# Kernel tuning notes

Measured on AMD Instinct MI355X. Metric: run time of the kernel, lower is better.

## Reference

```python
import jax, jax.numpy as jnp
import numpy as np

EPS = 1e-5
N_HEADS = 16
TOP_K = 2


def _ln(x, g, b):
    m = x.mean(-1, keepdims=True)
    v = ((x - m) ** 2).mean(-1, keepdims=True)
    return (x - m) / jnp.sqrt(v + EPS) * g + b


def _block_fwd(x, ln1_g, ln1_b, ln2_g, ln2_b, Wq, bq, Wk, bk, Wv, bv, Wo, bo,
               Wr, br, e_w1, e_b1, e_w2, e_b2):
    B, S, D = x.shape
    H = N_HEADS
    hd = D // H
    # --- LN + causal MHA + residual (dropout is identity at eval) ---
    h = _ln(x, ln1_g, ln1_b)
    q = (h @ Wq + bq).reshape(B, S, H, hd).transpose(0, 2, 1, 3)  # [B,H,S,hd]
    k = (h @ Wk + bk).reshape(B, S, H, hd).transpose(0, 2, 1, 3)
    v = (h @ Wv + bv).reshape(B, S, H, hd).transpose(0, 2, 1, 3)
    scores = jnp.einsum('bhqd,bhkd->bhqk', q, k) / (hd ** 0.5)
    causal = jnp.tril(jnp.ones((S, S), dtype=bool))
    scores = jnp.where(causal, scores, -jnp.inf)
    attn = jax.nn.softmax(scores, axis=-1)
    o = jnp.einsum('bhqk,bhkd->bhqd', attn, v).transpose(0, 2, 1, 3).reshape(B, S, D)
    a = (o @ Wo + bo) + x
    # --- LN + dense-computed SparseMoE + residual ---
    h2 = _ln(a, ln2_g, ln2_b)
    logits = h2 @ Wr + br                         # [B,S,E]
    topv = jax.lax.top_k(logits, TOP_K)[0]        # [B,S,K]
    kmask = logits >= topv[..., -1:]
    w = jax.nn.softmax(jnp.where(kmask, logits, -jnp.inf), axis=-1)  # [B,S,E]
    # dense per-expert FFN, exactly as the torch module computes it
    mid = jax.nn.gelu(jnp.einsum('bsd,edf->bsef', h2, e_w1) + e_b1,
                      approximate=False)          # [B,S,E,4D]
    eo = jnp.einsum('bsef,efd->bsed', mid, e_w2) + e_b2  # [B,S,E,D]
    moe = jnp.einsum('bse,bsed->bsd', w, eo)
    return moe + a


def setup_inputs() -> dict:
    key = jax.random.key(0)
    B, S, D, E = 1, 2048, 1024, 8
    F = 4 * D
    ks = jax.random.split(key, 8)

    def n(k, shape):
        return jax.random.normal(k, shape, jnp.float32) * 0.02

    return dict(
        x=jax.random.normal(ks[0], (B, S, D), jnp.float32),
        ln1_g=jnp.ones((D,), jnp.float32), ln1_b=jnp.zeros((D,), jnp.float32),
        ln2_g=jnp.ones((D,), jnp.float32), ln2_b=jnp.zeros((D,), jnp.float32),
        Wq=n(ks[1], (D, D)), bq=jnp.zeros((D,), jnp.float32),
        Wk=n(ks[2], (D, D)), bk=jnp.zeros((D,), jnp.float32),
        Wv=n(ks[3], (D, D)), bv=jnp.zeros((D,), jnp.float32),
        Wo=n(ks[4], (D, D)), bo=jnp.zeros((D,), jnp.float32),
        Wr=n(ks[5], (D, E)), br=jnp.zeros((E,), jnp.float32),
        e_w1=n(ks[6], (E, D, F)), e_b1=jnp.zeros((E, F), jnp.float32),
        e_w2=n(ks[7], (E, F, D)), e_b2=jnp.zeros((E, D), jnp.float32),
    )


def reference(x, ln1_g, ln1_b, ln2_g, ln2_b, Wq, bq, Wk, bk, Wv, bv, Wo, bo,
              Wr, br, e_w1, e_b1, e_w2, e_b2):
    return _block_fwd(x, ln1_g, ln1_b, ln2_g, ln2_b, Wq, bq, Wk, bk, Wv, bv,
                      Wo, bo, Wr, br, e_w1, e_b1, e_w2, e_b2)
```

## Files before the change

kernel.cpp:

```cpp
#include <hip/hip_runtime.h>
#include <hip/hip_bf16.h>
#include <math.h>

#define S 2048
#define Dm 1024
#define Ee 8
#define Ff 4096

typedef __attribute__((ext_vector_type(8))) short bf16x8;
typedef __attribute__((ext_vector_type(4))) float f32x4;

__device__ __forceinline__ unsigned short f2bf(float f) {
    union { float f; unsigned int u; } c; c.f = f;
    unsigned int r = (c.u + 0x7fffu + ((c.u >> 16) & 1u)) >> 16;
    return (unsigned short)r;
}

__device__ __forceinline__ void gload16(const void* g, void* l) {
    __builtin_amdgcn_global_load_lds(
        (const __attribute__((address_space(1))) void*)g,
        (__attribute__((address_space(3))) void*)l, 16, 0, 0);
}

__device__ __forceinline__ float gelu_f(float x) {
    float ax = fabsf(x) * 0.70710678118654752f;
    float t = 1.0f / (1.0f + 0.3275911f * ax);
    float p = t * (0.254829592f + t * (-0.284496736f + t * (1.421413741f +
              t * (-1.453152027f + t * 1.061405429f))));
    float er = 1.0f - p * __expf(-ax * ax);
    er = (x < 0.0f) ? -er : er;
    return 0.5f * x * (1.0f + er);
}

__global__ __launch_bounds__(256) void ln_kernel(const float* __restrict__ x,
                                                 const float* __restrict__ g,
                                                 const float* __restrict__ b,
                                                 unsigned short* __restrict__ obf) {
    int row = blockIdx.x;
    int tid = threadIdx.x;
    float4 v = ((const float4*)(x + (size_t)row * Dm))[tid];
    float s  = v.x + v.y + v.z + v.w;
    float sq = v.x*v.x + v.y*v.y + v.z*v.z + v.w*v.w;
    #pragma unroll
    for (int off = 1; off < 64; off <<= 1) {
        s  += __shfl_xor(s, off);
        sq += __shfl_xor(sq, off);
    }
    __shared__ float ps[4], pq[4];
    int wave = tid >> 6;
    if ((tid & 63) == 0) { ps[wave] = s; pq[wave] = sq; }
    __syncthreads();
    s  = ps[0] + ps[1] + ps[2] + ps[3];
    sq = pq[0] + pq[1] + pq[2] + pq[3];
    float mean = s * (1.0f / Dm);
    float var  = sq * (1.0f / Dm) - mean * mean;
    float rstd = rsqrtf(var + 1e-5f);
    float4 gv = ((const float4*)g)[tid];
    float4 bv = ((const float4*)b)[tid];
    float4 o;
    o.x = (v.x - mean) * rstd * gv.x + bv.x;
    o.y = (v.y - mean) * rstd * gv.y + bv.y;
    o.z = (v.z - mean) * rstd * gv.z + bv.z;
    o.w = (v.w - mean) * rstd * gv.w + bv.w;
    unsigned short t4[4] = { f2bf(o.x), f2bf(o.y), f2bf(o.z), f2bf(o.w) };
    *(uint2*)(obf + (size_t)row * Dm + tid * 4) = *(uint2*)t4;
}

__global__ __launch_bounds__(256) void ln2_fused(const float* __restrict__ x,
                                                 const float* __restrict__ p0,
                                                 const float* __restrict__ p1,
                                                 const float* __restrict__ bo,
                                                 const float* __restrict__ g,
                                                 const float* __restrict__ b,
                                                 const float* __restrict__ Wr,
                                                 const float* __restrict__ br,
                                                 float* __restrict__ aout,
                                                 unsigned short* __restrict__ h2b,
                                                 float* __restrict__ w_rt) {
    int row = blockIdx.x;
    int tid = threadIdx.x;
    size_t base = (size_t)row * Dm;
    float4 xv = ((const float4*)(x + base))[tid];
    float4 a0 = ((const float4*)(p0 + base))[tid];
    float4 a1 = ((const float4*)(p1 + base))[tid];
    float4 bv0 = ((const float4*)bo)[tid];
    float4 a;
    a.x = xv.x + a0.x + a1.x + bv0.x;
    a.y = xv.y + a0.y + a1.y + bv0.y;
    a.z = xv.z + a0.z + a1.z + bv0.z;
    a.w = xv.w + a0.w + a1.w + bv0.w;
    ((float4*)(aout + base))[tid] = a;
    float s  = a.x + a.y + a.z + a.w;
    float sq = a.x*a.x + a.y*a.y + a.z*a.z + a.w*a.w;
    #pragma unroll
    for (int off = 1; off < 64; off <<= 1) {
        s  += __shfl_xor(s, off);
        sq += __shfl_xor(sq, off);
    }
    __shared__ float ps[4], pq[4];
    int wave = tid >> 6;
    if ((tid & 63) == 0) { ps[wave] = s; pq[wave] = sq; }
    __syncthreads();
    s  = ps[0] + ps[1] + ps[2] + ps[3];
    sq = pq[0] + pq[1] + pq[2] + pq[3];
    float mean = s * (1.0f / Dm);
    float var  = sq * (1.0f / Dm) - mean * mean;
    float rstd = rsqrtf(var + 1e-5f);
    float4 gv = ((const float4*)g)[tid];
    float4 bbv = ((const float4*)b)[tid];
    float4 o;
    o.x = (a.x - mean) * rstd * gv.x + bbv.x;
    o.y = (a.y - mean) * rstd * gv.y + bbv.y;
    o.z = (a.z - mean) * rstd * gv.z + bbv.z;
    o.w = (a.w - mean) * rstd * gv.w + bbv.w;
    unsigned short t4[4] = { f2bf(o.x), f2bf(o.y), f2bf(o.z), f2bf(o.w) };
    *(uint2*)(h2b + base + tid * 4) = *(uint2*)t4;

    float lg[8];
    #pragma unroll
    for (int e = 0; e < 8; e++) lg[e] = 0.0f;
    float oc[4] = { o.x, o.y, o.z, o.w };
    #pragma unroll
    for (int c = 0; c < 4; c++) {
        const float4* wr4 = (const float4*)(Wr + (size_t)(tid * 4 + c) * Ee);
        float4 wa = wr4[0], wb = wr4[1];
        lg[0] += oc[c]*wa.x; lg[1] += oc[c]*wa.y; lg[2] += oc[c]*wa.z; lg[3] += oc[c]*wa.w;
        lg[4] += oc[c]*wb.x; lg[5] += oc[c]*wb.y; lg[6] += oc[c]*wb.z; lg[7] += oc[c]*wb.w;
    }
    #pragma unroll
    for (int e = 0; e < 8; e++)
        #pragma unroll
        for (int off = 1; off < 64; off <<= 1) lg[e] += __shfl_xor(lg[e], off);
    __shared__ float wlg[4][8];
    if ((tid & 63) == 0) {
        #pragma unroll
        for (int e = 0; e < 8; e++) wlg[wave][e] = lg[e];
    }
    __syncthreads();
    if (tid == 0) {
        float l8[8];
        #pragma unroll
        for (int e = 0; e < 8; e++) l8[e] = wlg[0][e] + wlg[1][e] + wlg[2][e] + wlg[3][e] + br[e];
        float v1 = -INFINITY, v2 = -INFINITY;
        for (int e = 0; e < 8; e++) {
            float xv2 = l8[e];
            if (xv2 > v1) { v2 = v1; v1 = xv2; }
            else if (xv2 > v2) v2 = xv2;
        }
        float wv[8]; float denom = 0.0f;
        for (int e = 0; e < 8; e++) {
            if (l8[e] >= v2) { wv[e] = __expf(l8[e] - v1); denom += wv[e]; }
            else wv[e] = 0.0f;
        }
        float inv = 1.0f / denom;
        for (int e = 0; e < 8; e++) w_rt[row * Ee + e] = wv[e] * inv;
    }
}

__global__ __launch_bounds__(256) void tconv(const float* __restrict__ src,
                                             unsigned short* __restrict__ dst,
                                             int Kk, int Nn) {
    src += (size_t)blockIdx.z * Kk * Nn;
    dst += (size_t)blockIdx.z * Kk * Nn;
    int n0 = blockIdx.x * 64, k0 = blockIdx.y * 64;
    int tid = threadIdx.x;
    __shared__ float t[64][65];
    #pragma unroll
    for (int p = 0; p < 4; p++) {
        int kr = p * 16 + (tid >> 4);
        int nc = (tid & 15) * 4;
        float4 v = *(const float4*)(src + (size_t)(k0 + kr) * Nn + n0 + nc);
        t[kr][nc] = v.x; t[kr][nc+1] = v.y; t[kr][nc+2] = v.z; t[kr][nc+3] = v.w;
    }
    __syncthreads();
    int nr = tid >> 2;
    int kc = (tid & 3) * 16;
    unsigned short o[16];
    #pragma unroll
    for (int j = 0; j < 16; j++) o[j] = f2bf(t[kc + j][nr]);
    *(bf16x8*)(dst + (size_t)(n0 + nr) * Kk + k0 + kc)     = *(bf16x8*)&o[0];
    *(bf16x8*)(dst + (size_t)(n0 + nr) * Kk + k0 + kc + 8) = *(bf16x8*)&o[8];
}

template<int MODE>
__global__ __launch_bounds__(256, 2) void gemm_db(const unsigned short* __restrict__ A,
                                                  const unsigned short* __restrict__ Wt,
                                                  const float* __restrict__ bias0,
                                                  const float* __restrict__ bias1,
                                                  const float* __restrict__ bias2,
                                                  void* __restrict__ Cout,
                                                  int M, int N, int K) {
    const int tid = threadIdx.x;
    const int lane = tid & 63;
    const int w = tid >> 6;
    const int lr = lane >> 4, lc = lane & 15;
    const int wr = w >> 1, wc = w & 1;

    int kc = (MODE == 1) ? blockIdx.z : 0;
    const int m0 = blockIdx.y * 128;
    const int n0 = blockIdx.x * 128;
    const int KL   = (MODE == 1) ? 512 : K;
    const int Koff = kc * KL;

    __shared__ __align__(16) unsigned short As[2][128 * 64];
    __shared__ __align__(16) unsigned short Bs[2][128 * 64];

    const int srow = lane >> 3;
    const int csw  = ((lane & 7) ^ srow) * 8;
    const unsigned short* asrc[4];
    const unsigned short* bsrc[4];
    #pragma unroll
    for (int i = 0; i < 4; i++) {
        int rl = w * 32 + i * 8 + srow;
        asrc[i] = A  + (size_t)(m0 + rl) * K + Koff + csw;
        bsrc[i] = Wt + (size_t)(n0 + rl) * K + Koff + csw;
    }

    f32x4 acc[4][4];
    #pragma unroll
    for (int a = 0; a < 4; a++)
        #pragma unroll
        for (int bb = 0; bb < 4; bb++) acc[a][bb] = (f32x4)0.0f;

    auto STAGE = [&](int buf, int kblk) {
        const size_t koff = (size_t)kblk * 64;
        #pragma unroll
        for (int i = 0; i < 4; i++) {
            gload16(asrc[i] + koff, &As[buf][(w * 32 + i * 8) * 64]);
            gload16(bsrc[i] + koff, &Bs[buf][(w * 32 + i * 8) * 64]);
        }
    };

    const int nt = KL / 64;
    STAGE(0, 0);
    for (int t = 0; t < nt; ++t) {
        const int cur = t & 1;
        if (t + 1 < nt) {
            STAGE(cur ^ 1, t + 1);
            asm volatile("s_waitcnt vmcnt(8)" ::: "memory");
        } else {
            asm volatile("s_waitcnt vmcnt(0)" ::: "memory");
        }
        __builtin_amdgcn_s_barrier();
        #pragma unroll
        for (int ks = 0; ks < 2; ks++) {
            const int ck = ((ks * 4 + lr) ^ (lc & 7)) * 8;
            bf16x8 af[4], bfv[4];
            #pragma unroll
            for (int fm = 0; fm < 4; fm++)
                af[fm] = *(const bf16x8*)&As[cur][(wr * 64 + fm * 16 + lc) * 64 + ck];
            #pragma unroll
            for (int fn = 0; fn < 4; fn++)
                bfv[fn] = *(const bf16x8*)&Bs[cur][(wc * 64 + fn * 16 + lc) * 64 + ck];
            #pragma unroll
            for (int fm = 0; fm < 4; fm++)
                #pragma unroll
                for (int fn = 0; fn < 4; fn++)
                    acc[fm][fn] = __builtin_amdgcn_mfma_f32_16x16x32_bf16(af[fm], bfv[fn], acc[fm][fn], 0, 0, 0);
        }
        asm volatile("" ::: "memory");
        __builtin_amdgcn_s_barrier();
    }

    #pragma unroll
    for (int fm = 0; fm < 4; fm++) {
        #pragma unroll
        for (int r = 0; r < 4; r++) {
            int m = m0 + wr * 64 + fm * 16 + lr * 4 + r;
            #pragma unroll
            for (int fn = 0; fn < 4; fn++) {
                int ncol = n0 + wc * 64 + fn * 16 + lc;
                float val = acc[fm][fn][r];
                if constexpr (MODE == 0) {
                    const float* bb = (ncol < 1024) ? bias0 : (ncol < 2048 ? bias1 : bias2);
                    val += bb[ncol & 1023];
                    ((unsigned short*)Cout)[(size_t)m * N + ncol] = f2bf(val);
                } else {
                    ((float*)Cout)[(size_t)kc * M * N + (size_t)m * N + ncol] = val;
                }
            }
        }
    }
}

template<int MODE>
__global__ __launch_bounds__(256, 4) void gemm_moe(const unsigned short* __restrict__ A,
                                                   const unsigned short* __restrict__ Wt,
                                                   const float* __restrict__ bias,
                                                   void* __restrict__ Cout,
                                                   const int* __restrict__ rows,
                                                   const int* __restrict__ counts,
                                                   const int* __restrict__ offs,
                                                   int N, int K) {
    const int tid = threadIdx.x;
    const int lane = tid & 63;
    const int w = tid >> 6;
    const int lr = lane >> 4, lc = lane & 15;
    const int wr = w >> 1, wc = w & 1;

    int e, kc;
    if constexpr (MODE == 2) { e = blockIdx.z; kc = 0; }
    else { e = blockIdx.z >> 2; kc = blockIdx.z & 3; }
    const int Mcnt = counts[e];
    const int m0 = blockIdx.y * 128;
    if (m0 >= Mcnt) return;
    const int n0 = blockIdx.x * 128;
    const int KL = (MODE == 3) ? (K >> 2) : K;
    const int Koff = kc * KL;
    const unsigned short* Wz = Wt + (size_t)e * N * K;
    const float* biasz = bias + (size_t)e * N;
    const int zoff = offs[e];

    __shared__ __align__(16) unsigned short As[128 * 64];
    __shared__ __align__(16) unsigned short Bs[128 * 64];

    const int srow = lane >> 3;
    const int csw  = ((lane & 7) ^ srow) * 8;
    const unsigned short* asrc[4];
    const unsigned short* bsrc[4];
    #pragma unroll
    for (int i = 0; i < 4; i++) {
        int rl = w * 32 + i * 8 + srow;
        int ma = m0 + rl;
        int srcRow;
        if constexpr (MODE == 2) srcRow = rows[e * S + (ma < Mcnt ? ma : Mcnt - 1)];
        else                     srcRow = zoff + (ma < Mcnt ? ma : Mcnt - 1);
        asrc[i] = A  + (size_t)srcRow * K + Koff + csw;
        bsrc[i] = Wz + (size_t)(n0 + rl) * K + Koff + csw;
    }

    f32x4 acc[4][4];
    #pragma unroll
    for (int a = 0; a < 4; a++)
        #pragma unroll
        for (int bb = 0; bb < 4; bb++) acc[a][bb] = (f32x4)0.0f;

    for (int k0 = 0; k0 < KL; k0 += 64) {
        #pragma unroll
        for (int i = 0; i < 4; i++) {
            gload16(asrc[i] + k0, &As[(w * 32 + i * 8) * 64]);
            gload16(bsrc[i] + k0, &Bs[(w * 32 + i * 8) * 64]);
        }
        __syncthreads();
        #pragma unroll
        for (int ks = 0; ks < 2; ks++) {
            const int ck = ((ks * 4 + lr) ^ (lc & 7)) * 8;
            bf16x8 af[4], bfv[4];
            #pragma unroll
            for (int fm = 0; fm < 4; fm++)
                af[fm] = *(const bf16x8*)&As[(wr * 64 + fm * 16 + lc) * 64 + ck];
            #pragma unroll
            for (int fn = 0; fn < 4; fn++)
                bfv[fn] = *(const bf16x8*)&Bs[(wc * 64 + fn * 16 + lc) * 64 + ck];
            #pragma unroll
            for (int fm = 0; fm < 4; fm++)
                #pragma unroll
                for (int fn = 0; fn < 4; fn++)
                    acc[fm][fn] = __builtin_amdgcn_mfma_f32_16x16x32_bf16(af[fm], bfv[fn], acc[fm][fn], 0, 0, 0);
        }
        __syncthreads();
    }

    #pragma unroll
    for (int fm = 0; fm < 4; fm++) {
        #pragma unroll
        for (int r = 0; r < 4; r++) {
            int m = m0 + wr * 64 + fm * 16 + lr * 4 + r;
            if (m >= Mcnt) continue;
            #pragma unroll
            for (int fn = 0; fn < 4; fn++) {
                int ncol = n0 + wc * 64 + fn * 16 + lc;
                float val = acc[fm][fn][r];
                if constexpr (MODE == 2) {
                    val += biasz[ncol];
                    ((unsigned short*)Cout)[(size_t)(zoff + m) * N + ncol] = f2bf(gelu_f(val));
                } else {
                    if (kc == 0) val += biasz[ncol];
                    ((float*)Cout)[(size_t)kc * 4096 * N + (size_t)(zoff + m) * N + ncol] = val;
                }
            }
        }
    }
}

__global__ __launch_bounds__(256) void attn_mfma(const unsigned short* __restrict__ qkv,
                                                 unsigned short* __restrict__ ob) {
    int qt = (int)gridDim.x - 1 - (int)blockIdx.x;
    int h  = blockIdx.y;
    int tid = threadIdx.x;
    int lane = tid & 63, w = tid >> 6;
    int lr = lane >> 4, lc = lane & 15;

    __shared__ __align__(16) unsigned short Kl[2][64 * 64];
    __shared__ __align__(16) unsigned short Vt[2][64 * 64];
    __shared__ __align__(16) unsigned short Pl[4][16 * 64];

    bf16x8 qf[2];
    int qg_base = qt * 64 + w * 16;
    {
        int qrow = qg_base + lc;
        #pragma unroll
        for (int ks = 0; ks < 2; ks++)
            qf[ks] = *(const bf16x8*)(qkv + (size_t)qrow * 3072 + h * 64 + ks * 32 + lr * 8);
    }

    const int srow = lane >> 3;
    const int scw  = ((lane & 7) ^ srow) * 8;
    const unsigned short* ksrc[2];
    #pragma unroll
    for (int i = 0; i < 2; i++)
        ksrc[i] = qkv + (size_t)(w * 16 + i * 8 + srow) * 3072 + h * 64 + 1024 + scw;
    int vrow[2], vcg[2];
    const unsigned short* vsrc[2];
    #pragma unroll
    for (int i = 0; i < 2; i++) {
        int u = tid + i * 256;
        vrow[i] = u >> 3; vcg[i] = (u & 7) * 8;
        vsrc[i] = qkv + (size_t)vrow[i] * 3072 + h * 64 + 2048 + vcg[i];
    }

    f32x4 oacc[4];
    #pragma unroll
    for (int fd = 0; fd < 4; fd++) oacc[fd] = (f32x4)0.0f;
    float mrun[4], lrun[4];
    #pragma unroll
    for (int r = 0; r < 4; r++) { mrun[r] = -INFINITY; lrun[r] = 0.0f; }

    bf16x8 vreg[2];
    vreg[0] = *(const bf16x8*)(vsrc[0]);
    vreg[1] = *(const bf16x8*)(vsrc[1]);
    gload16(ksrc[0], &Kl[0][(w * 16 + 0) * 64]);
    gload16(ksrc[1], &Kl[0][(w * 16 + 8) * 64]);
    #pragma unroll
    for (int i = 0; i < 2; i++)
        #pragma unroll
        for (int j = 0; j < 8; j++) {
            int d = vcg[i] + j;
            int ch = ((vrow[i] >> 3) ^ (d & 7) ^ (d >> 3)) & 7;
            Vt[0][d * 64 + ch * 8 + (vrow[i] & 7)] = (unsigned short)vreg[i][j];
        }
    __syncthreads();

    for (int kt = 0; kt <= qt; kt++) {
        const int cur = kt & 1;
        if (kt < qt) {
            size_t off = (size_t)(kt + 1) * 64 * 3072;
            vreg[0] = *(const bf16x8*)(vsrc[0] + off);
            vreg[1] = *(const bf16x8*)(vsrc[1] + off);
            gload16(ksrc[0] + off, &Kl[cur ^ 1][(w * 16 + 0) * 64]);
            gload16(ksrc[1] + off, &Kl[cur ^ 1][(w * 16 + 8) * 64]);
        }

        f32x4 sc[4];
        #pragma unroll
        for (int fn = 0; fn < 4; fn++) sc[fn] = (f32x4)0.0f;
        #pragma unroll
        for (int fn = 0; fn < 4; fn++)
            #pragma unroll
            for (int ks = 0; ks < 2; ks++) {
                bf16x8 kf = *(const bf16x8*)&Kl[cur][(fn * 16 + lc) * 64 + ((ks * 4 + lr) ^ (lc & 7)) * 8];
                sc[fn] = __builtin_amdgcn_mfma_f32_16x16x32_bf16(qf[ks], kf, sc[fn], 0, 0, 0);
            }

        float st[4][4];
        float mloc[4];
        #pragma unroll
        for (int r = 0; r < 4; r++) mloc[r] = -INFINITY;
        #pragma unroll
        for (int fn = 0; fn < 4; fn++)
            #pragma unroll
            for (int r = 0; r < 4; r++) {
                float sv = sc[fn][r] * 0.125f;
                if (kt == qt) {
                    int kvg = kt * 64 + fn * 16 + lc;
                    int qg  = qg_base + lr * 4 + r;
                    if (kvg > qg) sv = -INFINITY;
                }
                st[fn][r] = sv;
                mloc[r] = fmaxf(mloc[r], sv);
            }
        #pragma unroll
        for (int r = 0; r < 4; r++) {
            mloc[r] = fmaxf(mloc[r], __shfl_xor(mloc[r], 1));
            mloc[r] = fmaxf(mloc[r], __shfl_xor(mloc[r], 2));
            mloc[r] = fmaxf(mloc[r], __shfl_xor(mloc[r], 4));
            mloc[r] = fmaxf(mloc[r], __shfl_xor(mloc[r], 8));
        }
        float fsc[4], lpart[4];
        #pragma unroll
        for (int r = 0; r < 4; r++) {
            float mnew = fmaxf(mrun[r], mloc[r]);
            fsc[r] = __expf(mrun[r] - mnew);
            mrun[r] = mnew;
            lpart[r] = 0.0f;
        }
        float pv[4][4];
        #pragma unroll
        for (int fn = 0; fn < 4; fn++)
            #pragma unroll
            for (int r = 0; r < 4; r++) {
                pv[fn][r] = __expf(st[fn][r] - mrun[r]);
                lpart[r] += pv[fn][r];
            }
        #pragma unroll
        for (int r = 0; r < 4; r++) {
            lpart[r] += __shfl_xor(lpart[r], 1);
            lpart[r] += __shfl_xor(lpart[r], 2);
            lpart[r] += __shfl_xor(lpart[r], 4);
            lpart[r] += __shfl_xor(lpart[r], 8);
            lrun[r] = lrun[r] * fsc[r] + lpart[r];
        }
        #pragma unroll
        for (int fn = 0; fn < 4; fn++)
            #pragma unroll
            for (int r = 0; r < 4; r++) {
                int q = lr * 4 + r;
                int kvc = fn * 16 + lc;
                int ch = ((kvc >> 3) ^ (q & 7) ^ (q >> 3)) & 7;
                Pl[w][q * 64 + ch * 8 + (kvc & 7)] = f2bf(pv[fn][r]);
            }
        #pragma unroll
        for (int fd = 0; fd < 4; fd++)
            #pragma unroll
            for (int r = 0; r < 4; r++) oacc[fd][r] *= fsc[r];

        if (kt < qt) {
            #pragma unroll
            for (int i = 0; i < 2; i++)
                #pragma unroll
                for (int j = 0; j < 8; j++) {
                    int d = vcg[i] + j;
                    int ch = ((vrow[i] >> 3) ^ (d & 7) ^ (d >> 3)) & 7;
                    Vt[cur ^ 1][d * 64 + ch * 8 + (vrow[i] & 7)] = (unsigned short)vreg[i][j];
                }
        }

        __syncthreads();

        #pragma unroll
        for (int ks = 0; ks < 2; ks++) {
            int chp = ((ks * 4 + lr) ^ (lc & 7) ^ (lc >> 3)) & 7;
            bf16x8 pa = *(const bf16x8*)&Pl[w][lc * 64 + chp * 8];
            #pragma unroll
            for (int fd = 0; fd < 4; fd++) {
                int d = fd * 16 + lc;
                int chv = ((ks * 4 + lr) ^ (d & 7) ^ (d >> 3)) & 7;
                bf16x8 vb = *(const bf16x8*)&Vt[cur][d * 64 + chv * 8];
                oacc[fd] = __builtin_amdgcn_mfma_f32_16x16x32_bf16(pa, vb, oacc[fd], 0, 0, 0);
            }
        }
        __syncthreads();
    }
    #pragma unroll
    for (int fd = 0; fd < 4; fd++)
        #pragma unroll
        for (int r = 0; r < 4; r++) {
            float val = oacc[fd][r] / lrun[r];
            ob[(size_t)(qg_base + lr * 4 + r) * 1024 + h * 64 + fd * 16 + lc] = f2bf(val);
        }
}

__global__ __launch_bounds__(256) void listbuild_kernel(const float* __restrict__ w_rt,
                                                        int* __restrict__ rows,
                                                        int* __restrict__ counts,
                                                        int* __restrict__ offs,
                                                        int* __restrict__ tok2slot,
                                                        float* __restrict__ tokw) {
    int tid = threadIdx.x;
    __shared__ int sc[256];
    __shared__ int runoff_s;
    int ncnt[8];
    #pragma unroll
    for (int j = 0; j < 8; j++) ncnt[j] = 0;
    if (tid == 0) runoff_s = 0;
    __syncthreads();
    for (int e = 0; e < Ee; e++) {
        int t0 = tid * 8;
        int sel = 0, flags = 0;
        #pragma unroll
        for (int j = 0; j < 8; j++)
            if (w_rt[(size_t)(t0 + j) * Ee + e] > 0.0f) { flags |= 1 << j; sel++; }
        sc[tid] = sel;
        __syncthreads();
        for (int off = 1; off < 256; off <<= 1) {
            int add = (tid >= off) ? sc[tid - off] : 0;
            __syncthreads();
            sc[tid] += add;
            __syncthreads();
        }
        int base = runoff_s;
        int pos = sc[tid] - sel;
        #pragma unroll
        for (int j = 0; j < 8; j++) {
            if (flags & (1 << j)) {
                rows[e * S + pos] = t0 + j;
                int c = ncnt[j];
                if (c < 2) {
                    tok2slot[(t0 + j) * 2 + c] = base + pos;
                    tokw[(t0 + j) * 2 + c] = w_rt[(size_t)(t0 + j) * Ee + e];
                    ncnt[j] = c + 1;
                }
                pos++;
            }
        }
        __syncthreads();
        if (tid == 0) {
            offs[e] = base;
            counts[e] = sc[255];
            runoff_s = base + sc[255];
        }
        __syncthreads();
    }
}

__global__ __launch_bounds__(256) void combine_kernel(float* __restrict__ out,
                                                      const float* __restrict__ eo,
                                                      const int* __restrict__ tok2slot,
                                                      const float* __restrict__ tokw) {
    int t = blockIdx.x, d = threadIdx.x;
    int s0 = tok2slot[t * 2], s1 = tok2slot[t * 2 + 1];
    float w0 = tokw[t * 2], w1 = tokw[t * 2 + 1];
    float4 o = ((const float4*)(out + (size_t)t * Dm))[d];
    float ax = 0, ay = 0, az = 0, aw = 0, bx = 0, by = 0, bz = 0, bw = 0;
    #pragma unroll
    for (int p = 0; p < 4; p++) {
        const float* ep = eo + (size_t)p * 4096 * Dm;
        float4 a = ((const float4*)(ep + (size_t)s0 * Dm))[d];
        float4 b = ((const float4*)(ep + (size_t)s1 * Dm))[d];
        ax += a.x; ay += a.y; az += a.z; aw += a.w;
        bx += b.x; by += b.y; bz += b.z; bw += b.w;
    }
    o.x += w0 * ax + w1 * bx;
    o.y += w0 * ay + w1 * by;
    o.z += w0 * az + w1 * bz;
    o.w += w0 * aw + w1 * bw;
    ((float4*)(out + (size_t)t * Dm))[d] = o;
}

extern "C" void kernel_launch(void* const* d_in, const int* in_sizes, int n_in,
                              void* d_out, int out_size, void* d_ws, size_t ws_size,
                              hipStream_t stream) {
    const float* x    = (const float*)d_in[0];
    const float* ln1g = (const float*)d_in[1];
    const float* ln1b = (const float*)d_in[2];
    const float* ln2g = (const float*)d_in[3];
    const float* ln2b = (const float*)d_in[4];
    const float* Wq   = (const float*)d_in[5];
    const float* bq   = (const float*)d_in[6];
    const float* Wk   = (const float*)d_in[7];
    const float* bk   = (const float*)d_in[8];
    const float* Wv   = (const float*)d_in[9];
    const float* bv   = (const float*)d_in[10];
    const float* Wo   = (const float*)d_in[11];
    const float* bo   = (const float*)d_in[12];
    const float* Wr   = (const float*)d_in[13];
    const float* br   = (const float*)d_in[14];
    const float* ew1  = (const float*)d_in[15];
    const float* eb1  = (const float*)d_in[16];
    const float* ew2  = (const float*)d_in[17];
    const float* eb2  = (const float*)d_in[18];
    float* out = (float*)d_out;

    char* wsb = (char*)d_ws;
    const size_t MB = 1 << 20;
    unsigned short* ew1T = (unsigned short*)(wsb);
    float*          eo   = (float*)         (wsb);
    unsigned short* ew2T = (unsigned short*)(wsb + 64*MB);
    unsigned short* mid  = (unsigned short*)(wsb + 128*MB);
    unsigned short* qkvT = (unsigned short*)(wsb + 160*MB);
    unsigned short* WoT  = (unsigned short*)(wsb + 166*MB);
    unsigned short* h_bf = (unsigned short*)(wsb + 168*MB);
    unsigned short* qkv  = (unsigned short*)(wsb + 172*MB);
    float*          p01  = (float*)         (wsb + 168*MB);
    unsigned short* ob   = (unsigned short*)(wsb + 184*MB);
    unsigned short* h2b  = (unsigned short*)(wsb + 196*MB);
    float*          w_rt = (float*)         (wsb + 200*MB);
    int*            rows = (int*)           (wsb + 200*MB + 65536);
    int*            counts   = rows + Ee * S;
    int*            offs     = counts + Ee;
    int*            tok2slot = offs + Ee;
    float*          tokw     = (float*)(tok2slot + 2 * S);

    tconv<<<dim3(16, 16, 1), 256, 0, stream>>>(Wq, qkvT,               Dm, Dm);
    tconv<<<dim3(16, 16, 1), 256, 0, stream>>>(Wk, qkvT + 1024*1024,   Dm, Dm);
    tconv<<<dim3(16, 16, 1), 256, 0, stream>>>(Wv, qkvT + 2*1024*1024, Dm, Dm);
    tconv<<<dim3(16, 16, 1), 256, 0, stream>>>(Wo, WoT,                Dm, Dm);
    tconv<<<dim3(64, 16, 8), 256, 0, stream>>>(ew1, ew1T, Dm, Ff);
    tconv<<<dim3(16, 64, 8), 256, 0, stream>>>(ew2, ew2T, Ff, Dm);

    ln_kernel<<<S, 256, 0, stream>>>(x, ln1g, ln1b, h_bf);

    gemm_db<0><<<dim3(24, 16), 256, 0, stream>>>(h_bf, qkvT, bq, bk, bv,
        qkv, S, 3072, Dm);

    attn_mfma<<<dim3(32, 16), 256, 0, stream>>>(qkv, ob);

    gemm_db<1><<<dim3(8, 16, 2), 256, 0, stream>>>(ob, WoT, nullptr, nullptr, nullptr,
        p01, S, Dm, Dm);

    ln2_fused<<<S, 256, 0, stream>>>(x, p01, p01 + (size_t)S * Dm, bo, ln2g, ln2b,
                                     Wr, br, out, h2b, w_rt);
    listbuild_kernel<<<1, 256, 0, stream>>>(w_rt, rows, counts, offs, tok2slot, tokw);

    gemm_moe<2><<<dim3(32, 16, 8), 256, 0, stream>>>(h2b, ew1T, eb1,
        mid, rows, counts, offs, Ff, Dm);

    gemm_moe<3><<<dim3(8, 16, 32), 256, 0, stream>>>(mid, ew2T, eb2,
        eo, rows, counts, offs, Dm, Ff);

    combine_kernel<<<S, 256, 0, stream>>>(out, eo, tok2slot, tokw);
}
```

Before: 395.3 us.

## Store MoE split-K partials as bf16, remap MoE blocks by XCD, rebalance attention grid

The second expert GEMM now writes its four split-K partial outputs as bf16 instead of fp32, and the combine kernel reads and widens them. This halves the traffic for that intermediate buffer but rounds each partial to bf16 before summation. The expert GEMM blocks are remapped so consecutive block ids stay on the same XCD, which aims to improve L2 reuse. The attention grid is flattened and interleaves descending and ascending query tiles across head halves to balance causal work. It also raises wave priority around the MFMA sections and drops one barrier that sat before the PV product.

```diff
diff --git a/kernel.cpp b/kernel.cpp
--- a/kernel.cpp
+++ b/kernel.cpp
@@ -14,6 +14,10 @@
     union { float f; unsigned int u; } c; c.f = f;
     unsigned int r = (c.u + 0x7fffu + ((c.u >> 16) & 1u)) >> 16;
     return (unsigned short)r;
+}
+
+__device__ __forceinline__ float bf2f(unsigned short u) {
+    union { float f; unsigned int i; } c; c.i = ((unsigned int)u) << 16; return c.f;
 }
 
 __device__ __forceinline__ void gload16(const void* g, void* l) {
@@ -298,13 +302,25 @@
     const int lr = lane >> 4, lc = lane & 15;
     const int wr = w >> 1, wc = w & 1;
 
+    const int nx = gridDim.x, ny = gridDim.y;
+    const int nwg = nx * ny * gridDim.z;
+    int b = (int)blockIdx.x + nx * ((int)blockIdx.y + ny * (int)blockIdx.z);
+    {
+        int q = nwg >> 3, r = nwg & 7;
+        int xcd = b & 7, idx = b >> 3;
+        b = ((xcd < r) ? xcd * (q + 1) : r * (q + 1) + (xcd - r) * q) + idx;
+    }
+    const int by = b % ny;
+    const int bx = (b / ny) % nx;
+    const int bz = b / (ny * nx);
+
     int e, kc;
-    if constexpr (MODE == 2) { e = blockIdx.z; kc = 0; }
-    else { e = blockIdx.z >> 2; kc = blockIdx.z & 3; }
+    if constexpr (MODE == 2) { e = bz; kc = 0; }
+    else { e = bz >> 2; kc = bz & 3; }
     const int Mcnt = counts[e];
-    const int m0 = blockIdx.y * 128;
+    const int m0 = by * 128;
     if (m0 >= Mcnt) return;
-    const int n0 = blockIdx.x * 128;
+    const int n0 = bx * 128;
     const int KL = (MODE == 3) ? (K >> 2) : K;
     const int Koff = kc * KL;
     const unsigned short* Wz = Wt + (size_t)e * N * K;
@@ -376,7 +392,7 @@
                     ((unsigned short*)Cout)[(size_t)(zoff + m) * N + ncol] = f2bf(gelu_f(val));
                 } else {
                     if (kc == 0) val += biasz[ncol];
-                    ((float*)Cout)[(size_t)kc * 4096 * N + (size_t)(zoff + m) * N + ncol] = val;
+                    ((unsigned short*)Cout)[(size_t)kc * 4096 * N + (size_t)(zoff + m) * N + ncol] = f2bf(val);
                 }
             }
         }
@@ -385,8 +401,10 @@
 
 __global__ __launch_bounds__(256) void attn_mfma(const unsigned short* __restrict__ qkv,
                                                  unsigned short* __restrict__ ob) {
-    int qt = (int)gridDim.x - 1 - (int)blockIdx.x;
-    int h  = blockIdx.y;
+    int bid = blockIdx.x;
+    int qt, h;
+    if (bid < 256) { qt = 31 - (bid & 31); h = bid >> 5; }
+    else           { qt = bid & 31;        h = 8 + ((bid - 256) >> 5); }
     int tid = threadIdx.x;
     int lane = tid & 63, w = tid >> 6;
     int lr = lane >> 4, lc = lane & 15;
@@ -454,6 +472,7 @@
         f32x4 sc[4];
         #pragma unroll
         for (int fn = 0; fn < 4; fn++) sc[fn] = (f32x4)0.0f;
+        __builtin_amdgcn_s_setprio(1);
         #pragma unroll
         for (int fn = 0; fn < 4; fn++)
             #pragma unroll
@@ -461,6 +480,7 @@
                 bf16x8 kf = *(const bf16x8*)&Kl[cur][(fn * 16 + lc) * 64 + ((ks * 4 + lr) ^ (lc & 7)) * 8];
                 sc[fn] = __builtin_amdgcn_mfma_f32_16x16x32_bf16(qf[ks], kf, sc[fn], 0, 0, 0);
             }
+        __builtin_amdgcn_s_setprio(0);
 
         float st[4][4];
         float mloc[4];
@@ -535,8 +555,7 @@
                 }
         }
 
-        __syncthreads();
-
+        __builtin_amdgcn_s_setprio(1);
         #pragma unroll
         for (int ks = 0; ks < 2; ks++) {
             int chp = ((ks * 4 + lr) ^ (lc & 7) ^ (lc >> 3)) & 7;
@@ -549,6 +568,7 @@
                 oacc[fd] = __builtin_amdgcn_mfma_f32_16x16x32_bf16(pa, vb, oacc[fd], 0, 0, 0);
             }
         }
+        __builtin_amdgcn_s_setprio(0);
         __syncthreads();
     }
     #pragma unroll
@@ -614,26 +634,28 @@
 }
 
 __global__ __launch_bounds__(256) void combine_kernel(float* __restrict__ out,
-                                                      const float* __restrict__ eo,
+                                                      const unsigned short* __restrict__ eo,
                                                       const int* __restrict__ tok2slot,
                                                       const float* __restrict__ tokw) {
     int t = blockIdx.x, d = threadIdx.x;
     int s0 = tok2slot[t * 2], s1 = tok2slot[t * 2 + 1];
     float w0 = tokw[t * 2], w1 = tokw[t * 2 + 1];
     float4 o = ((const float4*)(out + (size_t)t * Dm))[d];
-    float ax = 0, ay = 0, az = 0, aw = 0, bx = 0, by = 0, bz = 0, bw = 0;
+    float a[4] = {0,0,0,0}, b[4] = {0,0,0,0};
     #pragma unroll
     for (int p = 0; p < 4; p++) {
-        const float* ep = eo + (size_t)p * 4096 * Dm;
-        float4 a = ((const float4*)(ep + (size_t)s0 * Dm))[d];
-        float4 b = ((const float4*)(ep + (size_t)s1 * Dm))[d];
-        ax += a.x; ay += a.y; az += a.z; aw += a.w;
-        bx += b.x; by += b.y; bz += b.z; bw += b.w;
-    }
-    o.x += w0 * ax + w1 * bx;
-    o.y += w0 * ay + w1 * by;
-    o.z += w0 * az + w1 * bz;
-    o.w += w0 * aw + w1 * bw;
+        const unsigned short* ep = eo + (size_t)p * 4096 * Dm;
+        uint2 ra = *(const uint2*)(ep + (size_t)s0 * Dm + d * 4);
+        uint2 rb = *(const uint2*)(ep + (size_t)s1 * Dm + d * 4);
+        const unsigned short* pa16 = (const unsigned short*)&ra;
+        const unsigned short* pb16 = (const unsigned short*)&rb;
+        #pragma unroll
+        for (int j = 0; j < 4; j++) { a[j] += bf2f(pa16[j]); b[j] += bf2f(pb16[j]); }
+    }
+    o.x += w0 * a[0] + w1 * b[0];
+    o.y += w0 * a[1] + w1 * b[1];
+    o.z += w0 * a[2] + w1 * b[2];
+    o.w += w0 * a[3] + w1 * b[3];
     ((float4*)(out + (size_t)t * Dm))[d] = o;
 }
 
@@ -664,7 +686,7 @@
     char* wsb = (char*)d_ws;
     const size_t MB = 1 << 20;
     unsigned short* ew1T = (unsigned short*)(wsb);
-    float*          eo   = (float*)         (wsb);
+    unsigned short* eo   = (unsigned short*)(wsb);
     unsigned short* ew2T = (unsigned short*)(wsb + 64*MB);
     unsigned short* mid  = (unsigned short*)(wsb + 128*MB);
     unsigned short* qkvT = (unsigned short*)(wsb + 160*MB);
@@ -693,7 +715,7 @@
     gemm_db<0><<<dim3(24, 16), 256, 0, stream>>>(h_bf, qkvT, bq, bk, bv,
         qkv, S, 3072, Dm);
 
-    attn_mfma<<<dim3(32, 16), 256, 0, stream>>>(qkv, ob);
+    attn_mfma<<<dim3(512, 1), 256, 0, stream>>>(qkv, ob);
 
     gemm_db<1><<<dim3(8, 16, 2), 256, 0, stream>>>(ob, WoT, nullptr, nullptr, nullptr,
         p01, S, Dm, Dm);
```

Result: no change. 402.1 us (+1.7%).
